# Optimization experiments

Measured on AMD Instinct MI355X. Metric: run time of the kernel, lower is better.

The kernel has to match this reference:

```python
import jax, jax.numpy as jnp
import numpy as np

B, Hdim, Wdim, C, HEADS, WS = 16, 112, 112, 128, 4, 7
VD = C
MLP_H = int(4.0 * VD)
EPS = 1e-5


def _layernorm(x, g, b):
    mu = jnp.mean(x, axis=-1, keepdims=True)
    var = jnp.mean(jnp.square(x - mu), axis=-1, keepdims=True)
    return (x - mu) * jax.lax.rsqrt(var + EPS) * g + b


def _rel_pos_index(ws):
    # static numpy computation, identical to the torch buffer
    coords = np.stack(np.meshgrid(np.arange(ws), np.arange(ws), indexing='ij'))  # (2, ws, ws)
    cf = coords.reshape(2, -1)                       # (2, N)
    rel = cf[:, :, None] - cf[:, None, :]            # (2, N, N)
    rel = rel.transpose(1, 2, 0).copy()              # (N, N, 2)
    rel[:, :, 0] += ws - 1
    rel[:, :, 1] += ws - 1
    rel[:, :, 0] *= 2 * ws - 1
    return jnp.asarray(rel.sum(-1))                  # (N, N) int


def setup_inputs() -> dict:
    key = jax.random.key(0)
    ks = jax.random.split(key, 10)
    nrm = lambda k, s: jax.random.normal(k, s, jnp.float32) * 0.02
    return {
        'x': jax.random.normal(ks[0], (B, Hdim * Wdim, C), jnp.float32),
        'v': jax.random.normal(ks[1], (B, Hdim * Wdim, C), jnp.float32),
        'norm1_g': jnp.ones((C,), jnp.float32), 'norm1_b': jnp.zeros((C,), jnp.float32),
        'normv_g': jnp.ones((C,), jnp.float32), 'normv_b': jnp.zeros((C,), jnp.float32),
        'q_w': nrm(ks[2], (C, C)), 'q_b': jnp.zeros((C,), jnp.float32),
        'kv_w': nrm(ks[3], (2 * C, C)), 'kv_b': jnp.zeros((2 * C,), jnp.float32),
        'rpb_table': nrm(ks[4], ((2 * WS - 1) ** 2, HEADS)),
        'proj_w': nrm(ks[5], (VD, VD)), 'proj_b': jnp.zeros((VD,), jnp.float32),
        'norm2_g': jnp.ones((VD,), jnp.float32), 'norm2_b': jnp.zeros((VD,), jnp.float32),
        'fc1_w': nrm(ks[6], (MLP_H, VD)), 'fc1_b': jnp.zeros((MLP_H,), jnp.float32),
        'fc2_w': nrm(ks[7], (VD, MLP_H)), 'fc2_b': jnp.zeros((VD,), jnp.float32),
        'H': Hdim, 'W': Wdim,
    }


def reference(x, v, norm1_g, norm1_b, normv_g, normv_b, q_w, q_b, kv_w, kv_b,
              rpb_table, proj_w, proj_b, norm2_g, norm2_b, fc1_w, fc1_b,
              fc2_w, fc2_b, H, W):
    Bsz, L, Cd = x.shape
    ws = WS
    heads = HEADS
    hd = Cd // heads
    scale = hd ** (-0.5)

    xs = _layernorm(x, norm1_g, norm1_b).reshape(Bsz, H, W, Cd)
    vs = _layernorm(v, normv_g, normv_b).reshape(Bsz, H, W, Cd)

    pad_b = (ws - H % ws) % ws
    pad_r = (ws - W % ws) % ws
    if pad_b or pad_r:
        xs = jnp.pad(xs, ((0, 0), (0, pad_b), (0, pad_r), (0, 0)))
        vs = jnp.pad(vs, ((0, 0), (0, pad_b), (0, pad_r), (0, 0)))
    Hp, Wp = H + pad_b, W + pad_r

    def part(t):  # window partition -> (nW*B, ws*ws, C)
        return t.reshape(Bsz, Hp // ws, ws, Wp // ws, ws, t.shape[-1]) \
                .transpose(0, 1, 3, 2, 4, 5).reshape(-1, ws * ws, t.shape[-1])

    xw = part(xs)
    vw = part(vs)
    N = ws * ws

    q = (xw @ q_w.T + q_b).reshape(-1, N, heads, hd).transpose(0, 2, 1, 3)   # (B_, h, N, d)
    kv = (vw @ kv_w.T + kv_b).reshape(-1, N, 2, heads, hd).transpose(2, 0, 3, 1, 4)
    k, vv = kv[0], kv[1]

    attn = jnp.einsum('bhnd,bhmd->bhnm', q * scale, k)
    rpi = _rel_pos_index(ws)
    bias = rpb_table[rpi.reshape(-1)].reshape(N, N, heads).transpose(2, 0, 1)  # (h, N, N)
    attn = jax.nn.softmax(attn + bias[None], axis=-1)

    out = jnp.einsum('bhnm,bhmd->bhnd', attn, vv).transpose(0, 2, 1, 3).reshape(-1, N, Cd)
    out = out @ proj_w.T + proj_b

    # window reverse
    out = out.reshape(Bsz, Hp // ws, Wp // ws, ws, ws, VD) \
             .transpose(0, 1, 3, 2, 4, 5).reshape(Bsz, Hp, Wp, VD)
    out = out[:, :H, :W, :].reshape(Bsz, H * W, VD)

    xo = out + x  # residual with pre-norm shortcut
    h = _layernorm(xo, norm2_g, norm2_b)
    h = jax.nn.gelu(h @ fc1_w.T + fc1_b, approximate=False)
    h = h @ fc2_w.T + fc2_b
    return xo + h
```

## Files before the change

### kernel.cpp

```cpp
#include <hip/hip_runtime.h>
#include <hip/hip_bf16.h>
#include <math.h>

typedef __hip_bfloat16 bf16;
typedef __hip_bfloat162 bf162;
typedef __attribute__((ext_vector_type(8))) short bf16x8;
typedef __attribute__((ext_vector_type(4))) short short4v;
typedef __attribute__((ext_vector_type(4))) float f32x4;

__device__ __forceinline__ float b2f(bf16 x){ return __bfloat162float(x); }
__device__ __forceinline__ bf16  f2b(float x){ return __float2bfloat16(x); }
__device__ __forceinline__ short f2bs(float x){ bf16 h = __float2bfloat16(x); return *(short*)&h; }

constexpr int kH = 112, kW = 112, kC = 128, kHeads = 4, kWS = 7;
constexpr int kN = 49, kHD = 32, kL = kH * kW;
constexpr int kWinElems = kN * kC;
constexpr int kMLP = 512;
constexpr float kEps = 1e-5f;
constexpr float kScale = 0.17677669529663687f;
constexpr int kAP = 136;
constexpr int kHP = 520;

__global__ __launch_bounds__(256) void k_cvt(
    const float* __restrict__ qw, const float* __restrict__ kvw,
    const float* __restrict__ pw, const float* __restrict__ w1,
    const float* __restrict__ w2, short* __restrict__ dst)
{
    const int i = blockIdx.x * 256 + threadIdx.x;
    float val;
    if (i < 16384)       val = qw[i];
    else if (i < 49152)  val = kvw[i - 16384];
    else if (i < 65536)  val = pw[i - 49152];
    else if (i < 131072) val = w1[i - 65536];
    else                 val = w2[i - 131072];
    dst[i] = f2bs(val);
}

__global__ __launch_bounds__(256) void k_ln_qkv_mfma(
    const float* __restrict__ x, const float* __restrict__ v,
    const float* __restrict__ n1g, const float* __restrict__ n1b,
    const float* __restrict__ nvg, const float* __restrict__ nvb,
    const short* __restrict__ qwb, const float* __restrict__ qb,
    const short* __restrict__ kvwb, const float* __restrict__ kvb,
    bf16* __restrict__ qo, bf16* __restrict__ ko, bf16* __restrict__ vo)
{
    __shared__ short Xs[32 * kAP], Vs[32 * kAP];
    const int tid = threadIdx.x, wave = tid >> 6, lane = tid & 63;
    const int quad = lane >> 4, l16 = lane & 15;
    const int row0 = blockIdx.x * 32;
    const int c0 = lane * 2;

    for (int n = wave; n < 32; n += 4) {
        const size_t r = (size_t)(row0 + n) * kC;
        const float2 xv = *(const float2*)(x + r + c0);
        const float2 vv = *(const float2*)(v + r + c0);
        float sx = xv.x + xv.y, qx = xv.x * xv.x + xv.y * xv.y;
        float sv = vv.x + vv.y, qv = vv.x * vv.x + vv.y * vv.y;
        #pragma unroll
        for (int off = 32; off > 0; off >>= 1) {
            sx += __shfl_xor(sx, off); qx += __shfl_xor(qx, off);
            sv += __shfl_xor(sv, off); qv += __shfl_xor(qv, off);
        }
        const float mux = sx * (1.f / kC);
        const float ivx = rsqrtf(qx * (1.f / kC) - mux * mux + kEps);
        const float muv = sv * (1.f / kC);
        const float ivv = rsqrtf(qv * (1.f / kC) - muv * muv + kEps);
        Xs[n * kAP + c0]     = f2bs((xv.x - mux) * ivx * n1g[c0] + n1b[c0]);
        Xs[n * kAP + c0 + 1] = f2bs((xv.y - mux) * ivx * n1g[c0 + 1] + n1b[c0 + 1]);
        Vs[n * kAP + c0]     = f2bs((vv.x - muv) * ivv * nvg[c0] + nvb[c0]);
        Vs[n * kAP + c0 + 1] = f2bs((vv.y - muv) * ivv * nvg[c0 + 1] + nvb[c0 + 1]);
    }
    __syncthreads();

    int woff[2];
    #pragma unroll
    for (int mt = 0; mt < 2; mt++) {
        const int gr = row0 + mt * 16 + l16;
        const int b = gr / kL, l = gr - b * kL;
        const int h = l / kW, w_ = l - h * kW;
        woff[mt] = ((b << 8) + (h / 7) * 16 + (w_ / 7)) * kWinElems
                 + ((h % 7) * 7 + (w_ % 7)) * kC;
    }

    bf16x8 xf[2][4], vf[2][4];
    #pragma unroll
    for (int mt = 0; mt < 2; mt++)
        #pragma unroll
        for (int ks = 0; ks < 4; ks++) {
            xf[mt][ks] = *(const bf16x8*)&Xs[(mt * 16 + l16) * kAP + ks * 32 + quad * 8];
            vf[mt][ks] = *(const bf16x8*)&Vs[(mt * 16 + l16) * kAP + ks * 32 + quad * 8];
        }

    #pragma unroll
    for (int j = 0; j < 6; j++) {
        const int nt = wave * 6 + j;
        const bool isq = (nt < 8);
        const short* wmat = isq ? qwb : kvwb;
        const int wr0 = (isq ? nt : nt - 8) * 16;
        const float* bias = isq ? qb : kvb;
        const int bidx = wr0 + quad * 4;
        f32x4 a0 = { bias[bidx], bias[bidx + 1], bias[bidx + 2], bias[bidx + 3] };
        f32x4 a1 = a0;
        if (isq) {
            #pragma unroll
            for (int ks = 0; ks < 4; ks++) {
                const bf16x8 af = *(const bf16x8*)(wmat + (size_t)(wr0 + l16) * kC + ks * 32 + quad * 8);
                a0 = __builtin_amdgcn_mfma_f32_16x16x32_bf16(af, xf[0][ks], a0, 0, 0, 0);
                a1 = __builtin_amdgcn_mfma_f32_16x16x32_bf16(af, xf[1][ks], a1, 0, 0, 0);
            }
        } else {
            #pragma unroll
            for (int ks = 0; ks < 4; ks++) {
                const bf16x8 af = *(const bf16x8*)(wmat + (size_t)(wr0 + l16) * kC + ks * 32 + quad * 8);
                a0 = __builtin_amdgcn_mfma_f32_16x16x32_bf16(af, vf[0][ks], a0, 0, 0, 0);
                a1 = __builtin_amdgcn_mfma_f32_16x16x32_bf16(af, vf[1][ks], a1, 0, 0, 0);
            }
        }
        bf16* dst = isq ? qo : (nt < 16 ? ko : vo);
        const int cb = (isq ? nt : (nt < 16 ? nt - 8 : nt - 16)) * 16 + quad * 4;
        short4v p0, p1;
        #pragma unroll
        for (int i = 0; i < 4; i++) { p0[i] = f2bs(a0[i]); p1[i] = f2bs(a1[i]); }
        *(short4v*)((short*)dst + (size_t)woff[0] + cb) = p0;
        *(short4v*)((short*)dst + (size_t)woff[1] + cb) = p1;
    }
}

__global__ __launch_bounds__(256, 3) void k_attn_mfma(
    bf16* __restrict__ qbuf, const bf16* __restrict__ kbuf,
    const bf16* __restrict__ vbuf, const float* __restrict__ rpb)
{
    __shared__ short Pl[kHeads][64 * 64];
    __shared__ short Vt[kHeads][32 * 64];
    __shared__ float rpl[kHeads][169];
    const int tid = threadIdx.x, wave = tid >> 6, lane = tid & 63;
    const int quad = lane >> 4, l16 = lane & 15;
    const int head = wave;
    const size_t wbase = (size_t)blockIdx.x * kWinElems;

    for (int i = lane; i < 169; i += 64) rpl[head][i] = rpb[i * kHeads + head];

    bf16x8 qf[4], kf[4];
    const bf16* qp = qbuf + wbase + head * kHD + quad * 8;
    const bf16* kp = kbuf + wbase + head * kHD + quad * 8;
    #pragma unroll
    for (int t = 0; t < 4; t++) {
        qf[t] = *(const bf16x8*)(qp + (size_t)(t * 16 + l16) * kC);
        kf[t] = *(const bf16x8*)(kp + (size_t)(t * 16 + l16) * kC);
    }

    #pragma unroll
    for (int h = 0; h < 4; h++) {
        for (int i = tid; i < 1024; i += 256) {
            const int m = i >> 4, d2 = (i & 15) << 1;
            int val = 0;
            if (m < 49) val = *(const int*)(vbuf + wbase + (size_t)m * kC + h * kHD + d2);
            Vt[h][d2 * 64 + (m ^ ((d2 & 7) << 3))]         = (short)(val & 0xffff);
            Vt[h][(d2 + 1) * 64 + (m ^ (((d2 + 1) & 7) << 3))] = (short)(val >> 16);
        }
    }

    f32x4 S[4][4];
    #pragma unroll
    for (int nt = 0; nt < 4; nt++)
        #pragma unroll
        for (int mt = 0; mt < 4; mt++)
            S[nt][mt] = __builtin_amdgcn_mfma_f32_16x16x32_bf16(
                qf[nt], kf[mt], (f32x4){0.f, 0.f, 0.f, 0.f}, 0, 0, 0);

    __syncthreads();

    int an[4][4];
    #pragma unroll
    for (int nt = 0; nt < 4; nt++)
        #pragma unroll
        for (int i = 0; i < 4; i++) {
            const int n = nt * 16 + quad * 4 + i;
            an[nt][i] = 13 * (n / 7) + (n % 7) + 84;
        }
    int bm[4]; bool mok[4];
    #pragma unroll
    for (int mt = 0; mt < 4; mt++) {
        const int m = mt * 16 + l16;
        bm[mt] = 13 * (m / 7) + (m % 7);
        mok[mt] = (m < 49);
    }

    const float* rp = rpl[head];
    #pragma unroll
    for (int nt = 0; nt < 4; nt++)
        #pragma unroll
        for (int i = 0; i < 4; i++) {
            float sv[4];
            #pragma unroll
            for (int mt = 0; mt < 4; mt++) {
                int idx = an[nt][i] - bm[mt];
                idx = ((unsigned)idx > 168u) ? 0 : idx;
                sv[mt] = mok[mt] ? (S[nt][mt][i] * kScale + rp[idx]) : -1e30f;
            }
            float mx = fmaxf(fmaxf(sv[0], sv[1]), fmaxf(sv[2], sv[3]));
            #pragma unroll
            for (int off = 1; off < 16; off <<= 1) mx = fmaxf(mx, __shfl_xor(mx, off));
            float e[4];
            float sum = 0.f;
            #pragma unroll
            for (int mt = 0; mt < 4; mt++) { e[mt] = __expf(sv[mt] - mx); sum += e[mt]; }
            #pragma unroll
            for (int off = 1; off < 16; off <<= 1) sum += __shfl_xor(sum, off);
            const float inv = 1.f / sum;
            const int prow = nt * 16 + quad * 4 + i;
            short* pr = &Pl[head][prow * 64];
            const int sw = (prow & 7) << 3;
            #pragma unroll
            for (int mt = 0; mt < 4; mt++)
                pr[(mt * 16 + l16) ^ sw] = f2bs(e[mt] * inv);
        }

    bf16x8 va[2][2], pb2[4][2];
    #pragma unroll
    for (int dt = 0; dt < 2; dt++)
        #pragma unroll
        for (int ks = 0; ks < 2; ks++) {
            const int r = dt * 16 + l16;
            va[dt][ks] = *(const bf16x8*)&Vt[head][r * 64 + ((ks * 32 + quad * 8) ^ ((r & 7) << 3))];
        }
    #pragma unroll
    for (int nt = 0; nt < 4; nt++)
        #pragma unroll
        for (int ks = 0; ks < 2; ks++) {
            const int r = nt * 16 + l16;
            pb2[nt][ks] = *(const bf16x8*)&Pl[head][r * 64 + ((ks * 32 + quad * 8) ^ ((r & 7) << 3))];
        }
    f32x4 o[2][4];
    #pragma unroll
    for (int dt = 0; dt < 2; dt++)
        #pragma unroll
        for (int nt = 0; nt < 4; nt++) {
            f32x4 a = __builtin_amdgcn_mfma_f32_16x16x32_bf16(
                va[dt][0], pb2[nt][0], (f32x4){0.f, 0.f, 0.f, 0.f}, 0, 0, 0);
            o[dt][nt] = __builtin_amdgcn_mfma_f32_16x16x32_bf16(
                va[dt][1], pb2[nt][1], a, 0, 0, 0);
        }

    #pragma unroll
    for (int nt = 0; nt < 4; nt++) {
        const int n = nt * 16 + l16;
        if (n < 49) {
            bf16* dst = qbuf + wbase + (size_t)n * kC + head * kHD + quad * 4;
            #pragma unroll
            for (int dt = 0; dt < 2; dt++) {
                short4v p;
                #pragma unroll
                for (int i = 0; i < 4; i++) p[i] = f2bs(o[dt][nt][i]);
                *(short4v*)(dst + dt * 16) = p;
            }
        }
    }
}

__global__ __launch_bounds__(256) void k_proj_mfma(
    const bf16* __restrict__ ao, const short* __restrict__ pwb,
    const float* __restrict__ pb, const float* __restrict__ x,
    float* __restrict__ out)
{
    __shared__ short As[32 * kAP];
    const int tid = threadIdx.x, wave = tid >> 6, lane = tid & 63;
    const int quad = lane >> 4, l16 = lane & 15;
    const int row0 = blockIdx.x * 32;
    const int c0 = lane * 2;

    for (int n = wave; n < 32; n += 4) {
        const int gr = row0 + n;
        const int b = gr / kL, l = gr - b * kL;
        const int h = l / kW, w_ = l - h * kW;
        const size_t off = (size_t)(((b << 8) + (h / 7) * 16 + (w_ / 7))) * kWinElems
                         + ((h % 7) * 7 + (w_ % 7)) * kC;
        *(int*)&As[n * kAP + c0] = *(const int*)((const short*)ao + off + c0);
    }
    __syncthreads();

    bf16x8 bfrag[2][4];
    #pragma unroll
    for (int mt = 0; mt < 2; mt++)
        #pragma unroll
        for (int ks = 0; ks < 4; ks++)
            bfrag[mt][ks] = *(const bf16x8*)&As[(mt * 16 + l16) * kAP + ks * 32 + quad * 8];

    #pragma unroll
    for (int j = 0; j < 2; j++) {
        const int nt = wave * 2 + j;
        const int cb = nt * 16 + quad * 4;
        f32x4 a0 = { pb[cb], pb[cb + 1], pb[cb + 2], pb[cb + 3] };
        f32x4 a1 = a0;
        #pragma unroll
        for (int ks = 0; ks < 4; ks++) {
            const bf16x8 af = *(const bf16x8*)(pwb + (size_t)(nt * 16 + l16) * kC + ks * 32 + quad * 8);
            a0 = __builtin_amdgcn_mfma_f32_16x16x32_bf16(af, bfrag[0][ks], a0, 0, 0, 0);
            a1 = __builtin_amdgcn_mfma_f32_16x16x32_bf16(af, bfrag[1][ks], a1, 0, 0, 0);
        }
        #pragma unroll
        for (int mt = 0; mt < 2; mt++) {
            const size_t gr = row0 + mt * 16 + l16;
            float4 res = *(const float4*)(x + gr * kC + cb);
            const f32x4 a = mt ? a1 : a0;
            res.x += a[0]; res.y += a[1]; res.z += a[2]; res.w += a[3];
            *(float4*)(out + gr * kC + cb) = res;
        }
    }
}

constexpr int kMT = 32;

__global__ __launch_bounds__(256, 4) void k_mlp_mfma(
    float* __restrict__ out,
    const float* __restrict__ g2, const float* __restrict__ b2v,
    const short* __restrict__ w1b, const float* __restrict__ bb1,
    const short* __restrict__ w2b, const float* __restrict__ bb2)
{
    __shared__ short LDSu[kMT * kHP];
    short* const A_s = LDSu;
    short* const H_s = LDSu;
    const int tid = threadIdx.x, wave = tid >> 6, lane = tid & 63;
    const int quad = lane >> 4, l16 = lane & 15;
    const size_t row0 = (size_t)blockIdx.x * kMT;
    const int c0 = lane * 2;

    const float gg0 = g2[c0], gg1 = g2[c0 + 1];
    const float bv0 = b2v[c0], bv1 = b2v[c0 + 1];
    float2 xv[8];
    #pragma unroll
    for (int it = 0; it < 8; it++)
        xv[it] = *(const float2*)(out + (row0 + wave + it * 4) * kC + c0);
    float s[8], q[8];
    #pragma unroll
    for (int it = 0; it < 8; it++) {
        s[it] = xv[it].x + xv[it].y;
        q[it] = xv[it].x * xv[it].x + xv[it].y * xv[it].y;
    }
    #pragma unroll
    for (int off = 32; off > 0; off >>= 1) {
        #pragma unroll
        for (int it = 0; it < 8; it++) {
            s[it] += __shfl_xor(s[it], off);
            q[it] += __shfl_xor(q[it], off);
        }
    }
    #pragma unroll
    for (int it = 0; it < 8; it++) {
        const int n = wave + it * 4;
        const float mu = s[it] * (1.f / kC);
        const float iv = rsqrtf(q[it] * (1.f / kC) - mu * mu + kEps);
        const short h0 = f2bs((xv[it].x - mu) * iv * gg0 + bv0);
        const short h1 = f2bs((xv[it].y - mu) * iv * gg1 + bv1);
        *(int*)&A_s[n * kAP + c0] =
            ((int)(unsigned short)h1 << 16) | (int)(unsigned short)h0;
    }
    __syncthreads();

    bf16x8 bfrag[2][4];
    #pragma unroll
    for (int mt = 0; mt < 2; mt++)
        #pragma unroll
        for (int ks = 0; ks < 4; ks++)
            bfrag[mt][ks] = *(const bf16x8*)&A_s[(mt * 16 + l16) * kAP + ks * 32 + quad * 8];
    __syncthreads();

    const short* wbase = w1b + (size_t)(wave * 128 + l16) * kC + quad * 8;
    auto loadw1 = [&](bf16x8* dst, int t) {
        #pragma unroll
        for (int ks = 0; ks < 4; ks++)
            dst[ks] = *(const bf16x8*)(wbase + (size_t)t * (16 * kC) + ks * 32);
    };
    auto mfma8 = [&](f32x4* a, const bf16x8* w) {
        #pragma unroll
        for (int ks = 0; ks < 4; ks++) {
            a[0] = __builtin_amdgcn_mfma_f32_16x16x32_bf16(w[ks], bfrag[0][ks], a[0], 0, 0, 0);
            a[1] = __builtin_amdgcn_mfma_f32_16x16x32_bf16(w[ks], bfrag[1][ks], a[1], 0, 0, 0);
        }
    };
    #pragma unroll
    for (int g = 0; g < 2; g++) {
        f32x4 acc[4][2];
        #pragma unroll
        for (int t = 0; t < 4; t++) {
            const float4 bi = *(const float4*)(bb1 + (wave * 8 + g * 4 + t) * 16 + quad * 4);
            acc[t][0] = (f32x4){ bi.x, bi.y, bi.z, bi.w };
            acc[t][1] = acc[t][0];
        }
        bf16x8 wA[4], wB[4];
        loadw1(wA, g * 4 + 0);
        loadw1(wB, g * 4 + 1);
        mfma8(acc[0], wA);
        loadw1(wA, g * 4 + 2);
        mfma8(acc[1], wB);
        loadw1(wB, g * 4 + 3);
        mfma8(acc[2], wA);
        mfma8(acc[3], wB);
        #pragma unroll
        for (int t = 0; t < 4; t++) {
            const int nb = (wave * 8 + g * 4 + t) * 16 + quad * 4;
            #pragma unroll
            for (int mt = 0; mt < 2; mt++) {
                short4v p;
                #pragma unroll
                for (int i = 0; i < 4; i++) {
                    const float a = acc[t][mt][i];
                    p[i] = f2bs(0.5f * a * (1.f + erff(a * 0.70710678118f)));
                }
                *(short4v*)&H_s[(mt * 16 + l16) * kHP + nb] = p;
            }
        }
    }
    __syncthreads();

    const int ct0 = wave * 2;
    f32x4 acc2[2][2];
    #pragma unroll
    for (int t = 0; t < 2; t++) {
        const float4 bi = *(const float4*)(bb2 + (ct0 + t) * 16 + quad * 4);
        acc2[t][0] = (f32x4){ bi.x, bi.y, bi.z, bi.w };
        acc2[t][1] = acc2[t][0];
    }
    const short* w2base = w2b + (size_t)(ct0 * 16 + l16) * kMLP + quad * 8;
    const short* hbase0 = &H_s[l16 * kHP + quad * 8];
    const short* hbase1 = &H_s[(16 + l16) * kHP + quad * 8];
    auto loadh = [&](bf16x8* h, bf16x8* w, int kk) {
        h[0] = *(const bf16x8*)(hbase0 + kk * 32);
        h[1] = *(const bf16x8*)(hbase1 + kk * 32);
        w[0] = *(const bf16x8*)(w2base + kk * 32);
        w[1] = *(const bf16x8*)(w2base + (size_t)16 * kMLP + kk * 32);
    };
    auto mfma4 = [&](const bf16x8* h, const bf16x8* w) {
        acc2[0][0] = __builtin_amdgcn_mfma_f32_16x16x32_bf16(w[0], h[0], acc2[0][0], 0, 0, 0);
        acc2[0][1] = __builtin_amdgcn_mfma_f32_16x16x32_bf16(w[0], h[1], acc2[0][1], 0, 0, 0);
        acc2[1][0] = __builtin_amdgcn_mfma_f32_16x16x32_bf16(w[1], h[0], acc2[1][0], 0, 0, 0);
        acc2[1][1] = __builtin_amdgcn_mfma_f32_16x16x32_bf16(w[1], h[1], acc2[1][1], 0, 0, 0);
    };
    bf16x8 hA[2], wwA[2], hB[2], wwB[2];
    loadh(hA, wwA, 0);
    #pragma unroll
    for (int kk = 0; kk < 16; kk += 2) {
        loadh(hB, wwB, kk + 1);
        mfma4(hA, wwA);
        if (kk + 2 < 16) loadh(hA, wwA, kk + 2);
        mfma4(hB, wwB);
    }

    #pragma unroll
    for (int t = 0; t < 2; t++) {
        const int cbv = (ct0 + t) * 16 + quad * 4;
        #pragma unroll
        for (int mt = 0; mt < 2; mt++) {
            const size_t m = row0 + mt * 16 + l16;
            float4 res = *(const float4*)(out + m * kC + cbv);
            res.x += acc2[t][mt][0]; res.y += acc2[t][mt][1];
            res.z += acc2[t][mt][2]; res.w += acc2[t][mt][3];
            *(float4*)(out + m * kC + cbv) = res;
        }
    }
}

extern "C" void kernel_launch(void* const* d_in, const int* in_sizes, int n_in,
                              void* d_out, int out_size, void* d_ws, size_t ws_size,
                              hipStream_t stream) {
    (void)in_sizes; (void)n_in; (void)out_size; (void)ws_size;
    const float* x      = (const float*)d_in[0];
    const float* v      = (const float*)d_in[1];
    const float* n1g    = (const float*)d_in[2];
    const float* n1b    = (const float*)d_in[3];
    const float* nvg    = (const float*)d_in[4];
    const float* nvb    = (const float*)d_in[5];
    const float* q_w    = (const float*)d_in[6];
    const float* q_b    = (const float*)d_in[7];
    const float* kv_w   = (const float*)d_in[8];
    const float* kv_b   = (const float*)d_in[9];
    const float* rpb    = (const float*)d_in[10];
    const float* proj_w = (const float*)d_in[11];
    const float* proj_b = (const float*)d_in[12];
    const float* n2g    = (const float*)d_in[13];
    const float* n2b    = (const float*)d_in[14];
    const float* fc1_w  = (const float*)d_in[15];
    const float* fc1_b  = (const float*)d_in[16];
    const float* fc2_w  = (const float*)d_in[17];
    const float* fc2_b  = (const float*)d_in[18];

    const size_t winTot = (size_t)4096 * kWinElems;
    bf16* qbuf = (bf16*)d_ws;
    bf16* kbuf = qbuf + winTot;
    bf16* vbuf = kbuf + winTot;
    short* wcvt = (short*)(vbuf + winTot);
    short* qwb  = wcvt;
    short* kvwb = qwb + 16384;
    short* pwb  = kvwb + 32768;
    short* w1b  = pwb + 16384;
    short* w2b  = w1b + 65536;
    float* outb = (float*)d_out;

    k_cvt<<<768, 256, 0, stream>>>(q_w, kv_w, proj_w, fc1_w, fc2_w, wcvt);
    k_ln_qkv_mfma<<<6272, 256, 0, stream>>>(x, v, n1g, n1b, nvg, nvb,
                                            qwb, q_b, kvwb, kv_b, qbuf, kbuf, vbuf);
    k_attn_mfma<<<4096, 256, 0, stream>>>(qbuf, kbuf, vbuf, rpb);
    k_proj_mfma<<<6272, 256, 0, stream>>>(qbuf, pwb, proj_b, x, outb);
    k_mlp_mfma<<<6272, 256, 0, stream>>>(outb, n2g, n2b, w1b, fc1_b, w2b, fc2_b);
}
```

Baseline: 746.8 us.

## Fuse output projection and MLP into one kernel with LDS-resident residual

Merges the projection kernel and the MLP kernel into a single kernel. The post-projection residual tile is kept in shared memory instead of being written to global memory and read back twice. This removes a full fp32 activation round-trip and one launch. In exchange LDS use per block grows, so the occupancy hint drops from 4 to 3 blocks.

New measurement: 726.4 us. -2.7%, faster.

```diff
diff --git a/kernel.cpp b/kernel.cpp
--- a/kernel.cpp
+++ b/kernel.cpp
@@ -20,6 +20,7 @@
 constexpr float kScale = 0.17677669529663687f;
 constexpr int kAP = 136;
 constexpr int kHP = 520;
+constexpr int kXP = 132;
 
 __global__ __launch_bounds__(256) void k_cvt(
     const float* __restrict__ qw, const float* __restrict__ kvw,
@@ -258,19 +259,28 @@
     }
 }
 
-__global__ __launch_bounds__(256) void k_proj_mfma(
+constexpr int kMT = 32;
+
+__global__ __launch_bounds__(256, 3) void k_proj_mlp(
     const bf16* __restrict__ ao, const short* __restrict__ pwb,
     const float* __restrict__ pb, const float* __restrict__ x,
-    float* __restrict__ out)
+    float* __restrict__ out,
+    const float* __restrict__ g2, const float* __restrict__ b2v,
+    const short* __restrict__ w1b, const float* __restrict__ bb1,
+    const short* __restrict__ w2b, const float* __restrict__ bb2)
 {
-    __shared__ short As[32 * kAP];
+    __shared__ float Xo[kMT * kXP];
+    __shared__ short U[kMT * kHP];
+    short* const As  = U;
+    short* const A_s = U;
+    short* const H_s = U;
     const int tid = threadIdx.x, wave = tid >> 6, lane = tid & 63;
     const int quad = lane >> 4, l16 = lane & 15;
-    const int row0 = blockIdx.x * 32;
+    const size_t row0 = (size_t)blockIdx.x * kMT;
     const int c0 = lane * 2;
 
     for (int n = wave; n < 32; n += 4) {
-        const int gr = row0 + n;
+        const int gr = (int)row0 + n;
         const int b = gr / kL, l = gr - b * kL;
         const int h = l / kW, w_ = l - h * kW;
         const size_t off = (size_t)(((b << 8) + (h / 7) * 16 + (w_ / 7))) * kWinElems
@@ -286,6 +296,14 @@
         for (int ks = 0; ks < 4; ks++)
             bfrag[mt][ks] = *(const bf16x8*)&As[(mt * 16 + l16) * kAP + ks * 32 + quad * 8];
 
+    float4 res[2][2];
+    #pragma unroll
+    for (int j = 0; j < 2; j++)
+        #pragma unroll
+        for (int mt = 0; mt < 2; mt++)
+            res[j][mt] = *(const float4*)(x + (row0 + mt * 16 + l16) * kC
+                                            + (wave * 2 + j) * 16 + quad * 4);
+
     #pragma unroll
     for (int j = 0; j < 2; j++) {
         const int nt = wave * 2 + j;
@@ -300,37 +318,20 @@
         }
         #pragma unroll
         for (int mt = 0; mt < 2; mt++) {
-            const size_t gr = row0 + mt * 16 + l16;
-            float4 res = *(const float4*)(x + gr * kC + cb);
             const f32x4 a = mt ? a1 : a0;
-            res.x += a[0]; res.y += a[1]; res.z += a[2]; res.w += a[3];
-            *(float4*)(out + gr * kC + cb) = res;
-        }
-    }
-}
-
-constexpr int kMT = 32;
-
-__global__ __launch_bounds__(256, 4) void k_mlp_mfma(
-    float* __restrict__ out,
-    const float* __restrict__ g2, const float* __restrict__ b2v,
-    const short* __restrict__ w1b, const float* __restrict__ bb1,
-    const short* __restrict__ w2b, const float* __restrict__ bb2)
-{
-    __shared__ short LDSu[kMT * kHP];
-    short* const A_s = LDSu;
-    short* const H_s = LDSu;
-    const int tid = threadIdx.x, wave = tid >> 6, lane = tid & 63;
-    const int quad = lane >> 4, l16 = lane & 15;
-    const size_t row0 = (size_t)blockIdx.x * kMT;
-    const int c0 = lane * 2;
+            float4 r = res[j][mt];
+            r.x += a[0]; r.y += a[1]; r.z += a[2]; r.w += a[3];
+            *(float4*)&Xo[(mt * 16 + l16) * kXP + cb] = r;
+        }
+    }
+    __syncthreads();
 
     const float gg0 = g2[c0], gg1 = g2[c0 + 1];
     const float bv0 = b2v[c0], bv1 = b2v[c0 + 1];
     float2 xv[8];
     #pragma unroll
     for (int it = 0; it < 8; it++)
-        xv[it] = *(const float2*)(out + (row0 + wave + it * 4) * kC + c0);
+        xv[it] = *(const float2*)&Xo[(wave + it * 4) * kXP + c0];
     float s[8], q[8];
     #pragma unroll
     for (int it = 0; it < 8; it++) {
@@ -357,12 +358,12 @@
     }
     __syncthreads();
 
-    bf16x8 bfrag[2][4];
+    bf16x8 bfrag2[2][4];
     #pragma unroll
     for (int mt = 0; mt < 2; mt++)
         #pragma unroll
         for (int ks = 0; ks < 4; ks++)
-            bfrag[mt][ks] = *(const bf16x8*)&A_s[(mt * 16 + l16) * kAP + ks * 32 + quad * 8];
+            bfrag2[mt][ks] = *(const bf16x8*)&A_s[(mt * 16 + l16) * kAP + ks * 32 + quad * 8];
     __syncthreads();
 
     const short* wbase = w1b + (size_t)(wave * 128 + l16) * kC + quad * 8;
@@ -374,8 +375,8 @@
     auto mfma8 = [&](f32x4* a, const bf16x8* w) {
         #pragma unroll
         for (int ks = 0; ks < 4; ks++) {
-            a[0] = __builtin_amdgcn_mfma_f32_16x16x32_bf16(w[ks], bfrag[0][ks], a[0], 0, 0, 0);
-            a[1] = __builtin_amdgcn_mfma_f32_16x16x32_bf16(w[ks], bfrag[1][ks], a[1], 0, 0, 0);
+            a[0] = __builtin_amdgcn_mfma_f32_16x16x32_bf16(w[ks], bfrag2[0][ks], a[0], 0, 0, 0);
+            a[1] = __builtin_amdgcn_mfma_f32_16x16x32_bf16(w[ks], bfrag2[1][ks], a[1], 0, 0, 0);
         }
     };
     #pragma unroll
@@ -452,10 +453,11 @@
         #pragma unroll
         for (int mt = 0; mt < 2; mt++) {
             const size_t m = row0 + mt * 16 + l16;
-            float4 res = *(const float4*)(out + m * kC + cbv);
-            res.x += acc2[t][mt][0]; res.y += acc2[t][mt][1];
-            res.z += acc2[t][mt][2]; res.w += acc2[t][mt][3];
-            *(float4*)(out + m * kC + cbv) = res;
+            const float4 xo = *(const float4*)&Xo[(mt * 16 + l16) * kXP + cbv];
+            float4 r;
+            r.x = xo.x + acc2[t][mt][0]; r.y = xo.y + acc2[t][mt][1];
+            r.z = xo.z + acc2[t][mt][2]; r.w = xo.w + acc2[t][mt][3];
+            *(float4*)(out + m * kC + cbv) = r;
         }
     }
 }
@@ -500,6 +502,6 @@
     k_ln_qkv_mfma<<<6272, 256, 0, stream>>>(x, v, n1g, n1b, nvg, nvb,
                                             qwb, q_b, kvwb, kv_b, qbuf, kbuf, vbuf);
     k_attn_mfma<<<4096, 256, 0, stream>>>(qbuf, kbuf, vbuf, rpb);
-    k_proj_mfma<<<6272, 256, 0, stream>>>(qbuf, pwb, proj_b, x, outb);
-    k_mlp_mfma<<<6272, 256, 0, stream>>>(outb, n2g, n2b, w1b, fc1_b, w2b, fc2_b);
+    k_proj_mlp<<<6272, 256, 0, stream>>>(qbuf, pwb, proj_b, x, outb,
+                                         n2g, n2b, w1b, fc1_b, w2b, fc2_b);
 }
```
